# Kernel tuning notes

Measured on AMD Instinct MI355X. Metric: run time of the kernel, lower is better.

## Reference

```python
import jax, jax.numpy as jnp
import numpy as np

B, N = 1024, 512
NUM_SCALARS = 7  # 7x0e
HID = 128


def setup_inputs() -> dict:
    key = jax.random.key(0)
    k1, k2, k3, k4, k5 = jax.random.split(key, 5)
    feats = jax.random.normal(k1, (B, N, NUM_SCALARS), dtype=jnp.float32)
    coors = jax.random.normal(k2, (B, N, 3), dtype=jnp.float32)
    adj_mat = jnp.zeros((B, N, N), dtype=jnp.bool_)
    # e3nn TP weights: standard normal, shape (mul_in1 * mul_in2 * mul_out,) = (7,)
    W_tp = jax.random.normal(k3, (NUM_SCALARS,), dtype=jnp.float32)
    # nn.Linear default init: U(-1/sqrt(fan_in), 1/sqrt(fan_in))
    lim1 = 1.0 / np.sqrt(3.0)
    W1 = jax.random.uniform(k4, (HID, 3), jnp.float32, -lim1, lim1)
    b1 = jnp.zeros((HID,), jnp.float32)
    lim2 = 1.0 / np.sqrt(HID)
    W2 = jax.random.uniform(k5, (3, HID), jnp.float32, -lim2, lim2)
    b2 = jnp.zeros((3,), jnp.float32)
    return {"feats": feats, "coors": coors, "adj_mat": adj_mat,
            "W_tp": W_tp, "W1": W1, "b1": b1, "W2": W2, "b2": b2}


def reference(feats, coors, adj_mat, W_tp, W1, b1, W2, b2):
    # FullyConnectedTensorProduct 7x0e (x) 1x1e -> 1x1e.
    # Single path: scalar channels mix into the vector; with component irrep
    # normalization the sqrt(3) cancels the 1/sqrt(3) of w3j(0,1,1), leaving a
    # fan-in normalization 1/sqrt(7).
    alpha = 1.0 / jnp.sqrt(jnp.asarray(feats.shape[-1], feats.dtype))
    s = jnp.einsum('bni,i->bn', feats, W_tp)  # [B, N]
    feats_out = alpha * s[..., None] * coors  # [B, N, 3]
    graph_embedding = feats_out.mean(axis=1)  # [B, 3]
    h = jax.nn.relu(graph_embedding @ W1.T + b1)  # [B, 128]
    return h @ W2.T + b2  # [B, 3]
```

## Files before the change

kernel.cpp:

```cpp
#include <hip/hip_runtime.h>


#define BLOCK 256
#define NSC 7
#define HID 128

__global__ __launch_bounds__(BLOCK) void dipole_e3nn_kernel(
    const float* __restrict__ feats,
    const float* __restrict__ coors,
    const float* __restrict__ W_tp,
    const float* __restrict__ W1,
    const float* __restrict__ b1,
    const float* __restrict__ W2,
    const float* __restrict__ b2,
    float* __restrict__ out,
    int N)
{
    const int b = blockIdx.x;
    const int t = threadIdx.x;
    const int wave = t >> 6;
    const int lane = t & 63;

    const float w0 = W_tp[0], w1 = W_tp[1], w2 = W_tp[2], w3 = W_tp[3],
                w4 = W_tp[4], w5 = W_tp[5], w6 = W_tp[6];

    const float* fb = feats + (size_t)b * N * NSC;
    const float* cb = coors + (size_t)b * N * 3;

    float ax = 0.f, ay = 0.f, az = 0.f;
    for (int n = t; n < N; n += BLOCK) {
        const float* f = fb + n * NSC;
        float s = f[0]*w0 + f[1]*w1 + f[2]*w2 + f[3]*w3
                + f[4]*w4 + f[5]*w5 + f[6]*w6;
        const float* c = cb + n * 3;
        ax += s * c[0];
        ay += s * c[1];
        az += s * c[2];
    }

    __shared__ float red[3][4];
    __shared__ float ge[3];
    #pragma unroll
    for (int off = 32; off > 0; off >>= 1) {
        ax += __shfl_down(ax, off);
        ay += __shfl_down(ay, off);
        az += __shfl_down(az, off);
    }
    if (lane == 0) { red[0][wave] = ax; red[1][wave] = ay; red[2][wave] = az; }
    __syncthreads();
    if (t == 0) {
        const float alpha = 0.3779644730092272f;
        const float scale = alpha / (float)N;
        ge[0] = (red[0][0] + red[0][1] + red[0][2] + red[0][3]) * scale;
        ge[1] = (red[1][0] + red[1][1] + red[1][2] + red[1][3]) * scale;
        ge[2] = (red[2][0] + red[2][1] + red[2][2] + red[2][3]) * scale;
    }
    __syncthreads();

    float p0 = 0.f, p1 = 0.f, p2 = 0.f;
    if (t < HID) {
        float h = ge[0] * W1[t*3 + 0] + ge[1] * W1[t*3 + 1] + ge[2] * W1[t*3 + 2] + b1[t];
        h = fmaxf(h, 0.f);
        p0 = h * W2[0*HID + t];
        p1 = h * W2[1*HID + t];
        p2 = h * W2[2*HID + t];
    }
    #pragma unroll
    for (int off = 32; off > 0; off >>= 1) {
        p0 += __shfl_down(p0, off);
        p1 += __shfl_down(p1, off);
        p2 += __shfl_down(p2, off);
    }
    if (lane == 0) { red[0][wave] = p0; red[1][wave] = p1; red[2][wave] = p2; }
    __syncthreads();
    if (t == 0) {
        out[b*3 + 0] = red[0][0] + red[0][1] + red[0][2] + red[0][3] + b2[0];
        out[b*3 + 1] = red[1][0] + red[1][1] + red[1][2] + red[1][3] + b2[1];
        out[b*3 + 2] = red[2][0] + red[2][1] + red[2][2] + red[2][3] + b2[2];
    }
}

extern "C" void kernel_launch(void* const* d_in, const int* in_sizes, int n_in,
                              void* d_out, int out_size, void* d_ws, size_t ws_size,
                              hipStream_t stream) {
    const float* feats = (const float*)d_in[0];
    const float* coors = (const float*)d_in[1];
    const float* W_tp  = (const float*)d_in[3];
    const float* W1    = (const float*)d_in[4];
    const float* b1    = (const float*)d_in[5];
    const float* W2    = (const float*)d_in[6];
    const float* b2    = (const float*)d_in[7];
    float* out = (float*)d_out;

    const int B = 1024;
    const int N = 512;

    dipole_e3nn_kernel<<<B, BLOCK, 0, stream>>>(feats, coors, W_tp, W1, b1, W2, b2, out, N);
}
```

Before: 11.61 us.

## Load two nodes per thread with float2 vectors and hoist MLP weight loads

Each thread now handles exactly two consecutive nodes, reading their features and coordinates as float2 vectors instead of looping over strided scalar loads. N is hard-coded to 512, which lets the kernel drop the loop and the division by N. The MLP weight and bias loads are issued at kernel start so their latency overlaps the feature loads, and the final reduction sums only the two waves that hold hidden units. The kernel no longer works for other values of N.

```diff
diff --git a/kernel.cpp b/kernel.cpp
--- a/kernel.cpp
+++ b/kernel.cpp
@@ -2,7 +2,6 @@
 
 
 #define BLOCK 256
-#define NSC 7
 #define HID 128
 
 __global__ __launch_bounds__(BLOCK) void dipole_e3nn_kernel(
@@ -13,30 +12,37 @@
     const float* __restrict__ b1,
     const float* __restrict__ W2,
     const float* __restrict__ b2,
-    float* __restrict__ out,
-    int N)
+    float* __restrict__ out)
 {
     const int b = blockIdx.x;
     const int t = threadIdx.x;
     const int wave = t >> 6;
     const int lane = t & 63;
 
+    const float2* fq = (const float2*)feats + (size_t)b * 1792 + t * 7;
+    const float2* cq = (const float2*)coors + (size_t)b * 768 + t * 3;
+
+    const float2 f0 = fq[0], f1 = fq[1], f2v = fq[2], f3 = fq[3],
+                 f4v = fq[4], f5 = fq[5], f6 = fq[6];
+    const float2 c0 = cq[0], c1 = cq[1], c2 = cq[2];
+
     const float w0 = W_tp[0], w1 = W_tp[1], w2 = W_tp[2], w3 = W_tp[3],
                 w4 = W_tp[4], w5 = W_tp[5], w6 = W_tp[6];
 
-    const float* fb = feats + (size_t)b * N * NSC;
-    const float* cb = coors + (size_t)b * N * 3;
+    float w1x = 0.f, w1y = 0.f, w1z = 0.f, bb1 = 0.f;
+    float w2a = 0.f, w2b = 0.f, w2c = 0.f;
+    if (t < HID) {
+        w1x = W1[t*3 + 0]; w1y = W1[t*3 + 1]; w1z = W1[t*3 + 2];
+        bb1 = b1[t];
+        w2a = W2[0*HID + t]; w2b = W2[1*HID + t]; w2c = W2[2*HID + t];
+    }
 
-    float ax = 0.f, ay = 0.f, az = 0.f;
-    for (int n = t; n < N; n += BLOCK) {
-        const float* f = fb + n * NSC;
-        float s = f[0]*w0 + f[1]*w1 + f[2]*w2 + f[3]*w3
-                + f[4]*w4 + f[5]*w5 + f[6]*w6;
-        const float* c = cb + n * 3;
-        ax += s * c[0];
-        ay += s * c[1];
-        az += s * c[2];
-    }
+    const float s0 = f0.x*w0 + f0.y*w1 + f1.x*w2 + f1.y*w3 + f2v.x*w4 + f2v.y*w5 + f3.x*w6;
+    const float s1 = f3.y*w0 + f4v.x*w1 + f4v.y*w2 + f5.x*w3 + f5.y*w4 + f6.x*w5 + f6.y*w6;
+
+    float ax = s0*c0.x + s1*c1.y;
+    float ay = s0*c0.y + s1*c2.x;
+    float az = s0*c1.x + s1*c2.y;
 
     __shared__ float red[3][4];
     __shared__ float ge[3];
@@ -50,7 +56,7 @@
     __syncthreads();
     if (t == 0) {
         const float alpha = 0.3779644730092272f;
-        const float scale = alpha / (float)N;
+        const float scale = alpha / 512.0f;
         ge[0] = (red[0][0] + red[0][1] + red[0][2] + red[0][3]) * scale;
         ge[1] = (red[1][0] + red[1][1] + red[1][2] + red[1][3]) * scale;
         ge[2] = (red[2][0] + red[2][1] + red[2][2] + red[2][3]) * scale;
@@ -59,11 +65,11 @@
 
     float p0 = 0.f, p1 = 0.f, p2 = 0.f;
     if (t < HID) {
-        float h = ge[0] * W1[t*3 + 0] + ge[1] * W1[t*3 + 1] + ge[2] * W1[t*3 + 2] + b1[t];
+        float h = ge[0]*w1x + ge[1]*w1y + ge[2]*w1z + bb1;
         h = fmaxf(h, 0.f);
-        p0 = h * W2[0*HID + t];
-        p1 = h * W2[1*HID + t];
-        p2 = h * W2[2*HID + t];
+        p0 = h * w2a;
+        p1 = h * w2b;
+        p2 = h * w2c;
     }
     #pragma unroll
     for (int off = 32; off > 0; off >>= 1) {
@@ -74,9 +80,9 @@
     if (lane == 0) { red[0][wave] = p0; red[1][wave] = p1; red[2][wave] = p2; }
     __syncthreads();
     if (t == 0) {
-        out[b*3 + 0] = red[0][0] + red[0][1] + red[0][2] + red[0][3] + b2[0];
-        out[b*3 + 1] = red[1][0] + red[1][1] + red[1][2] + red[1][3] + b2[1];
-        out[b*3 + 2] = red[2][0] + red[2][1] + red[2][2] + red[2][3] + b2[2];
+        out[b*3 + 0] = red[0][0] + red[0][1] + b2[0];
+        out[b*3 + 1] = red[1][0] + red[1][1] + b2[1];
+        out[b*3 + 2] = red[2][0] + red[2][1] + b2[2];
     }
 }
 
@@ -93,7 +99,5 @@
     float* out = (float*)d_out;
 
     const int B = 1024;
-    const int N = 512;
-
-    dipole_e3nn_kernel<<<B, BLOCK, 0, stream>>>(feats, coors, W_tp, W1, b1, W2, b2, out, N);
+    dipole_e3nn_kernel<<<B, BLOCK, 0, stream>>>(feats, coors, W_tp, W1, b1, W2, b2, out);
 }
```

Measured after the change: 10.84 us. 6.6% less time.
